# Optimization experiments

Hardware: AMD Instinct MI355X
Metric: run time of the kernel (lower is better)

## Reference

```python
import jax, jax.numpy as jnp
import numpy as np

EPS = 1e-12

def _l2norm(x):
    n = jnp.sqrt(jnp.sum(x * x, axis=-1, keepdims=True))
    return x / jnp.maximum(n, EPS)

def setup_inputs() -> dict:
    key = jax.random.key(0)
    k1, k2 = jax.random.split(key)
    B, S, H = 32, 256, 768
    return {
        "query_embs": jax.random.normal(k1, (B, S, H), dtype=jnp.float32),
        "key_embs": jax.random.normal(k2, (B, S, H), dtype=jnp.float32),
        "q_mask": jnp.ones((B, S), dtype=jnp.float32),
        "k_mask": jnp.ones((B, S), dtype=jnp.float32),
        "alpha_raw": jnp.asarray(1.0, dtype=jnp.float32),
        "logit_scale": jnp.asarray(0.0, dtype=jnp.float32),  # log(1.0)
    }

def reference(query_embs, key_embs, q_mask, k_mask, alpha_raw, logit_scale):
    # query_embs, key_embs: (B, S, H); masks: (B, S)
    S = query_embs.shape[1]
    q = _l2norm(query_embs)
    k = _l2norm(key_embs)
    # all-pairs token similarity: (B, B, S, T)
    sim = jnp.einsum('ish,jth->ijst', q, k)
    # distance-decay weighting (do_distance=True, exp_decay=True)
    alpha = jax.nn.softplus(alpha_raw)
    pos = jnp.arange(S, dtype=jnp.float32)
    dist = jnp.abs(pos[:, None] - pos[None, :])  # (S, S)
    sim = sim * jnp.exp(-alpha * dist)
    # validity mask: (B, B, S, T)
    valid = (q_mask[:, None, :, None] * k_mask[None, :, None, :]) > 0
    scale = jnp.exp(logit_scale)
    neg_inf = jnp.float32(-jnp.inf)
    logits = jnp.where(valid, scale * sim, neg_inf)
    all_inf = jnp.all(logits == neg_inf, axis=-1, keepdims=True)
    safe_logits = jnp.where(all_inf, 0.0, logits)
    p = jax.nn.softmax(safe_logits, axis=-1)
    p = jnp.where(all_inf, 0.0, p)
    # softmax-weighted key aggregation: (B, B, S, H)
    agg = jnp.einsum('ijst,jth->ijsh', p, k)
    # per-token cosine score, masked mean over query tokens
    scores = jnp.einsum('ish,ijsh->ijs', q, agg) * q_mask[:, None, :]
    denom = jnp.clip(jnp.sum(q_mask, axis=-1, keepdims=True), 1.0, None)
    return jnp.sum(scores, axis=-1) / denom  # (B, B)
```

## Files before the change

kernel.cpp:

```cpp
#include <hip/hip_runtime.h>
#include <cmath>

#define BB 32
#define SS 256
#define HH 768

typedef __attribute__((ext_vector_type(8))) short bfrag8;
typedef __attribute__((ext_vector_type(4))) float accf4;

__device__ __forceinline__ unsigned short f2bf(float x) {
    unsigned int b = __float_as_uint(x);
    return (unsigned short)((b + 0x7FFFu + ((b >> 16) & 1u)) >> 16);
}


__global__ __launch_bounds__(256)
void zero_kernel(float* __restrict__ Ksum) {
    Ksum[blockIdx.x * 256 + threadIdx.x] = 0.f;
}

__global__ __launch_bounds__(256)
void normcvt_kernel(const float* __restrict__ Q, const float* __restrict__ K,
                    const float* __restrict__ kmask,
                    float* __restrict__ invq, float* __restrict__ invk,
                    unsigned short* __restrict__ qws, unsigned short* __restrict__ kws,
                    float* __restrict__ Ksum) {
    __shared__ float sK[4 * HH];
    const int wave = threadIdx.x >> 6, lane = threadIdx.x & 63;
    const bool isQ = blockIdx.x < 2048;
    const int rr = (blockIdx.x * 4 + wave) & 8191;
    const float4* src4 = isQ ? (const float4*)(Q + (size_t)rr * HH)
                             : (const float4*)(K + (size_t)rr * HH);
    float4 vv[3]; float s = 0.f;
#pragma unroll
    for (int c = 0; c < 3; ++c) {
        vv[c] = src4[lane + 64 * c];
        s += vv[c].x * vv[c].x + vv[c].y * vv[c].y + vv[c].z * vv[c].z + vv[c].w * vv[c].w;
    }
#pragma unroll
    for (int off = 1; off < 64; off <<= 1) s += __shfl_xor(s, off);
    float inv = 1.f / fmaxf(sqrtf(s), 1e-12f);
    if (lane == 0) (isQ ? invq : invk)[rr] = inv;

    const int b = rr >> 8, srow = rr & 255;
    unsigned short* dst = isQ ? qws : kws;
    float m = 0.f;
    if (!isQ) m = (kmask[b * SS + srow] > 0.f) ? 1.f : 0.f;
    const int fp8 = (((((lane & 7) >> 1)) ^ ((srow >> 1) & 3)) << 3) + (lane & 1) * 4;
#pragma unroll
    for (int c = 0; c < 3; ++c) {
        int kc = (lane >> 3) + 8 * c;
        float4 n4;
        n4.x = vv[c].x * inv; n4.y = vv[c].y * inv; n4.z = vv[c].z * inv; n4.w = vv[c].w * inv;
        ushort4 o;
        o.x = f2bf(n4.x); o.y = f2bf(n4.y); o.z = f2bf(n4.z); o.w = f2bf(n4.w);
        *(ushort4*)(dst + (((size_t)b * 24 + kc) * 256 + srow) * 32 + fp8) = o;
        if (!isQ)
            *(float4*)(sK + wave * HH + (lane + 64 * c) * 4) =
                make_float4(n4.x * m, n4.y * m, n4.z * m, n4.w * m);
    }
    if (!isQ) {
        __syncthreads();
        const int j = ((int)blockIdx.x - 2048) >> 6;
        for (int e = threadIdx.x; e < HH; e += 256) {
            float v = sK[e] + sK[HH + e] + sK[2 * HH + e] + sK[3 * HH + e];
            atomicAdd(&Ksum[j * HH + e], v);
        }
    }
}

__global__ __launch_bounds__(256, 3)
void mfma_kernel(const unsigned short* __restrict__ qws, const unsigned short* __restrict__ kws,
                 const float* __restrict__ qmask, const float* __restrict__ kmask,
                 const float* __restrict__ araw_p, const float* __restrict__ lscale_p,
                 const float* __restrict__ Ksum, float* __restrict__ out) {
    __shared__ short lq[8192];
    __shared__ short lk[8192];
    __shared__ short lKsum[768];
    __shared__ float sKm[256];
    __shared__ float wtab[13];
    __shared__ float sRed[4][2];
    __shared__ float sPart[4];
    __shared__ float sKcnt, sQden;

    const int tid = threadIdx.x;
    const int lane = tid & 63, w = tid >> 6;
    const int quad = lane >> 4, col = lane & 15;
    const int i = blockIdx.x >> 5, j = blockIdx.x & 31;

    const float alpha = log1pf(__expf(araw_p[0]));
    const float scale = __expf(lscale_p[0]);

    float aq = qmask[i * SS + tid];
    float km = kmask[j * SS + tid];
    sKm[tid] = km;
    float c = (km > 0.f) ? 1.f : 0.f;
#pragma unroll
    for (int off = 1; off < 64; off <<= 1) { aq += __shfl_xor(aq, off); c += __shfl_xor(c, off); }
    if (lane == 0) { sRed[w][0] = aq; sRed[w][1] = c; }
    if (tid < 13) wtab[tid] = __expf(-alpha * (float)tid);
    if (tid < 192) {
        float4 kv = ((const float4*)(Ksum + (size_t)j * HH))[tid];
        ushort4 o;
        o.x = f2bf(kv.x); o.y = f2bf(kv.y); o.z = f2bf(kv.z); o.w = f2bf(kv.w);
        ((ushort4*)lKsum)[tid] = o;
    }
    __syncthreads();
    if (tid == 0) {
        sQden = fmaxf(sRed[0][0] + sRed[1][0] + sRed[2][0] + sRed[3][0], 1.f);
        sKcnt = sRed[0][1] + sRed[1][1] + sRed[2][1] + sRed[3][1];
    }

    accf4 acc[4][3];
    accf4 accB[4];
#pragma unroll
    for (int a = 0; a < 4; ++a) {
        accB[a] = (accf4)0.f;
#pragma unroll
        for (int b = 0; b < 3; ++b) acc[a][b] = (accf4)0.f;
    }

    const size_t qb0 = (size_t)i * 24 * 8192;
    const size_t kb0 = (size_t)j * 24 * 8192;
    const int perm8 = ((quad ^ ((col >> 1) & 3)) << 3);
    const unsigned short* qsrc = qws + qb0 + w * 2048 + lane * 8;
    const unsigned short* ksrc = kws + kb0 + w * 2048 + lane * 8;
    unsigned short* lqd = (unsigned short*)lq + w * 2048 + lane * 8;
    unsigned short* lkd = (unsigned short*)lk + w * 2048 + lane * 8;

    bfrag8 pq[4], pk[4];
#pragma unroll
    for (int n = 0; n < 4; ++n) {
        pq[n] = *(const bfrag8*)(qsrc + n * 512);
        pk[n] = *(const bfrag8*)(ksrc + n * 512);
    }

    for (int kc = 0; kc < 24; ++kc) {
        __syncthreads();
#pragma unroll
        for (int n = 0; n < 4; ++n) {
            *(bfrag8*)(lqd + n * 512) = pq[n];
            *(bfrag8*)(lkd + n * 512) = pk[n];
        }
        {
            const size_t noff = (size_t)((kc < 23) ? kc + 1 : 23) * 8192;
#pragma unroll
            for (int n = 0; n < 4; ++n) {
                pq[n] = *(const bfrag8*)(qsrc + noff + n * 512);
                pk[n] = *(const bfrag8*)(ksrc + noff + n * 512);
            }
        }
        __syncthreads();

        const bfrag8 kfrag = *(const bfrag8*)(lKsum + kc * 32 + quad * 8);
        bfrag8 bfr[6];
#pragma unroll
        for (int u = 0; u < 6; ++u) {
            int tb = 4 * w - 1 + u;
            if (tb >= 0 && tb <= 15)
                bfr[u] = *(const bfrag8*)(lk + (size_t)(tb * 16 + col) * 32 + perm8);
        }
#pragma unroll
        for (int sbl = 0; sbl < 4; ++sbl) {
            bfrag8 af = *(const bfrag8*)(lq + (size_t)((4 * w + sbl) * 16 + col) * 32 + perm8);
            accB[sbl] = __builtin_amdgcn_mfma_f32_16x16x32_bf16(af, kfrag, accB[sbl], 0, 0, 0);
#pragma unroll
            for (int dtb = 0; dtb < 3; ++dtb) {
                int tb = 4 * w + sbl - 1 + dtb;
                if (tb >= 0 && tb <= 15)
                    acc[sbl][dtb] = __builtin_amdgcn_mfma_f32_16x16x32_bf16(
                        af, bfr[sbl + dtb], acc[sbl][dtb], 0, 0, 0);
            }
        }
    }

    __syncthreads();
    const float kcnt = sKcnt;
    float part = 0.f;
#pragma unroll
    for (int sbl = 0; sbl < 4; ++sbl) {
        const int sbase = (4 * w + sbl) * 16 + quad * 4;
        float ns[4] = {0.f, 0.f, 0.f, 0.f}, ds[4] = {0.f, 0.f, 0.f, 0.f};
#pragma unroll
        for (int dtb = 0; dtb < 3; ++dtb) {
            int tb = 4 * w + sbl - 1 + dtb;
            if (tb < 0 || tb > 15) continue;
            int t = tb * 16 + col;
            float kmv = sKm[t];
#pragma unroll
            for (int reg = 0; reg < 4; ++reg) {
                int st = sbase + reg;
                int d = t - st;
                bool ok = (d >= -11) && (d <= 12) && (kmv > 0.f);
                int idx = d < 0 ? -d : d;
                idx = ok ? idx : 0;
                float raw = acc[sbl][dtb][reg];
                float e = ok ? expm1f(scale * raw * wtab[idx]) : 0.f;
                ns[reg] = fmaf(e, raw, ns[reg]);
                ds[reg] += e;
            }
        }
#pragma unroll
        for (int off = 1; off < 16; off <<= 1) {
#pragma unroll
            for (int reg = 0; reg < 4; ++reg) {
                ns[reg] += __shfl_xor(ns[reg], off);
                ds[reg] += __shfl_xor(ds[reg], off);
            }
        }
        if (col == 0) {
#pragma unroll
            for (int reg = 0; reg < 4; ++reg) {
                int st = sbase + reg;
                float qm = qmask[i * SS + st];
                float bse = accB[sbl][reg];
                float dtot = ds[reg] + kcnt;
                float v = (qm > 0.f && kcnt > 0.f) ? qm * (ns[reg] + bse) / dtot : 0.f;
                part += v;
            }
        }
    }
    part += __shfl_xor(part, 16);
    part += __shfl_xor(part, 32);
    if (lane == 0) sPart[w] = part;
    __syncthreads();
    if (tid == 0) out[i * BB + j] = (sPart[0] + sPart[1] + sPart[2] + sPart[3]) / sQden;
}


extern "C" void kernel_launch(void* const* d_in, const int* in_sizes, int n_in,
                              void* d_out, int out_size, void* d_ws, size_t ws_size,
                              hipStream_t stream) {
    const float* Q      = (const float*)d_in[0];
    const float* K      = (const float*)d_in[1];
    const float* qmask  = (const float*)d_in[2];
    const float* kmask  = (const float*)d_in[3];
    const float* araw   = (const float*)d_in[4];
    const float* lscale = (const float*)d_in[5];
    float* outp = (float*)d_out;

    float* invq  = (float*)d_ws;
    float* invk  = invq + 8192;
    float* Ksum  = invk + 8192;
    unsigned short* qws = (unsigned short*)(Ksum + 24576);
    unsigned short* kws = qws + 6291456;

    zero_kernel<<<96, 256, 0, stream>>>(Ksum);
    normcvt_kernel<<<4096, 256, 0, stream>>>(Q, K, kmask, invq, invk, qws, kws, Ksum);
    mfma_kernel<<<1024, 256, 0, stream>>>(qws, kws, qmask, kmask, araw, lscale, Ksum, outp);
}
```

Before: 163.2 us.

## Load MFMA fragments directly from global memory, dropping LDS staging

```diff
diff --git a/kernel.cpp b/kernel.cpp
--- a/kernel.cpp
+++ b/kernel.cpp
@@ -46,7 +46,7 @@
     unsigned short* dst = isQ ? qws : kws;
     float m = 0.f;
     if (!isQ) m = (kmask[b * SS + srow] > 0.f) ? 1.f : 0.f;
-    const int fp8 = (((((lane & 7) >> 1)) ^ ((srow >> 1) & 3)) << 3) + (lane & 1) * 4;
+    const int fp8 = (lane & 7) * 4;
 #pragma unroll
     for (int c = 0; c < 3; ++c) {
         int kc = (lane >> 3) + 8 * c;
@@ -73,9 +73,8 @@
 void mfma_kernel(const unsigned short* __restrict__ qws, const unsigned short* __restrict__ kws,
                  const float* __restrict__ qmask, const float* __restrict__ kmask,
                  const float* __restrict__ araw_p, const float* __restrict__ lscale_p,
-                 const float* __restrict__ Ksum, float* __restrict__ out) {
-    __shared__ short lq[8192];
-    __shared__ short lk[8192];
+                 const float* __restrict__ Ksum, const unsigned short* __restrict__ zpg,
+                 float* __restrict__ out) {
     __shared__ short lKsum[768];
     __shared__ float sKm[256];
     __shared__ float wtab[13];
@@ -120,58 +119,48 @@
         for (int b = 0; b < 3; ++b) acc[a][b] = (accf4)0.f;
     }
 
-    const size_t qb0 = (size_t)i * 24 * 8192;
-    const size_t kb0 = (size_t)j * 24 * 8192;
-    const int perm8 = ((quad ^ ((col >> 1) & 3)) << 3);
-    const unsigned short* qsrc = qws + qb0 + w * 2048 + lane * 8;
-    const unsigned short* ksrc = kws + kb0 + w * 2048 + lane * 8;
-    unsigned short* lqd = (unsigned short*)lq + w * 2048 + lane * 8;
-    unsigned short* lkd = (unsigned short*)lk + w * 2048 + lane * 8;
-
-    bfrag8 pq[4], pk[4];
-#pragma unroll
-    for (int n = 0; n < 4; ++n) {
-        pq[n] = *(const bfrag8*)(qsrc + n * 512);
-        pk[n] = *(const bfrag8*)(ksrc + n * 512);
-    }
-
+    const int lo = col * 32 + quad * 8;
+    const unsigned short* qp = qws + (size_t)i * 24 * 8192 + (4 * w) * 512 + lo;
+    const unsigned short* kb[6];
+    int kstep[6];
+#pragma unroll
+    for (int u = 0; u < 6; ++u) {
+        int tb = 4 * w - 1 + u;
+        bool inb = (tb >= 0) && (tb <= 15);
+        kb[u] = inb ? (kws + (size_t)j * 24 * 8192 + tb * 512 + lo) : (zpg + lo);
+        kstep[u] = inb ? 8192 : 0;
+    }
+
+    bfrag8 cq[4], ck[6];
+#pragma unroll
+    for (int n = 0; n < 4; ++n) cq[n] = *(const bfrag8*)(qp + n * 512);
+#pragma unroll
+    for (int u = 0; u < 6; ++u) ck[u] = *(const bfrag8*)(kb[u]);
+
+#pragma unroll
     for (int kc = 0; kc < 24; ++kc) {
-        __syncthreads();
-#pragma unroll
-        for (int n = 0; n < 4; ++n) {
-            *(bfrag8*)(lqd + n * 512) = pq[n];
-            *(bfrag8*)(lkd + n * 512) = pk[n];
-        }
-        {
-            const size_t noff = (size_t)((kc < 23) ? kc + 1 : 23) * 8192;
-#pragma unroll
-            for (int n = 0; n < 4; ++n) {
-                pq[n] = *(const bfrag8*)(qsrc + noff + n * 512);
-                pk[n] = *(const bfrag8*)(ksrc + noff + n * 512);
-            }
-        }
-        __syncthreads();
+        const int kn = (kc < 23) ? kc + 1 : 23;
+        bfrag8 nq[4], nk[6];
+#pragma unroll
+        for (int n = 0; n < 4; ++n)
+            nq[n] = *(const bfrag8*)(qp + (size_t)kn * 8192 + n * 512);
+#pragma unroll
+        for (int u = 0; u < 6; ++u)
+            nk[u] = *(const bfrag8*)(kb[u] + (size_t)kn * (size_t)kstep[u]);
 
         const bfrag8 kfrag = *(const bfrag8*)(lKsum + kc * 32 + quad * 8);
-        bfrag8 bfr[6];
-#pragma unroll
-        for (int u = 0; u < 6; ++u) {
-            int tb = 4 * w - 1 + u;
-            if (tb >= 0 && tb <= 15)
-                bfr[u] = *(const bfrag8*)(lk + (size_t)(tb * 16 + col) * 32 + perm8);
-        }
 #pragma unroll
         for (int sbl = 0; sbl < 4; ++sbl) {
-            bfrag8 af = *(const bfrag8*)(lq + (size_t)((4 * w + sbl) * 16 + col) * 32 + perm8);
-            accB[sbl] = __builtin_amdgcn_mfma_f32_16x16x32_bf16(af, kfrag, accB[sbl], 0, 0, 0);
-#pragma unroll
-            for (int dtb = 0; dtb < 3; ++dtb) {
-                int tb = 4 * w + sbl - 1 + dtb;
-                if (tb >= 0 && tb <= 15)
-                    acc[sbl][dtb] = __builtin_amdgcn_mfma_f32_16x16x32_bf16(
-                        af, bfr[sbl + dtb], acc[sbl][dtb], 0, 0, 0);
-            }
-        }
+            accB[sbl] = __builtin_amdgcn_mfma_f32_16x16x32_bf16(cq[sbl], kfrag, accB[sbl], 0, 0, 0);
+#pragma unroll
+            for (int dtb = 0; dtb < 3; ++dtb)
+                acc[sbl][dtb] = __builtin_amdgcn_mfma_f32_16x16x32_bf16(
+                    cq[sbl], ck[sbl + dtb], acc[sbl][dtb], 0, 0, 0);
+        }
+#pragma unroll
+        for (int n = 0; n < 4; ++n) cq[n] = nq[n];
+#pragma unroll
+        for (int u = 0; u < 6; ++u) ck[u] = nk[u];
     }
 
     __syncthreads();
@@ -242,10 +231,12 @@
     float* invq  = (float*)d_ws;
     float* invk  = invq + 8192;
     float* Ksum  = invk + 8192;
-    unsigned short* qws = (unsigned short*)(Ksum + 24576);
+    float* zpgf  = Ksum + 24576;
+    unsigned short* qws = (unsigned short*)(zpgf + 256);
     unsigned short* kws = qws + 6291456;
 
-    zero_kernel<<<96, 256, 0, stream>>>(Ksum);
+    zero_kernel<<<97, 256, 0, stream>>>(Ksum);
     normcvt_kernel<<<4096, 256, 0, stream>>>(Q, K, kmask, invq, invk, qws, kws, Ksum);
-    mfma_kernel<<<1024, 256, 0, stream>>>(qws, kws, qmask, kmask, araw, lscale, Ksum, outp);
-}
+    mfma_kernel<<<1024, 256, 0, stream>>>(qws, kws, qmask, kmask, araw, lscale,
+                                          Ksum, (const unsigned short*)zpgf, outp);
+}
```

Measured after the change: 188.0 us. 1.15x slower.

## Double-buffer LDS tiles with direct global-to-LDS loads in MFMA kernel

Applied to the files above, without the earlier changes.

```diff
diff --git a/kernel.cpp b/kernel.cpp
--- a/kernel.cpp
+++ b/kernel.cpp
@@ -11,6 +11,11 @@
 __device__ __forceinline__ unsigned short f2bf(float x) {
     unsigned int b = __float_as_uint(x);
     return (unsigned short)((b + 0x7FFFu + ((b >> 16) & 1u)) >> 16);
+}
+
+__device__ __forceinline__ void gload16(const void* g, void* l) {
+    __builtin_amdgcn_global_load_lds((const __attribute__((address_space(1))) void*)g,
+                                     (__attribute__((address_space(3))) void*)l, 16, 0, 0);
 }
 
 
@@ -69,13 +74,13 @@
     }
 }
 
-__global__ __launch_bounds__(256, 3)
+__global__ __launch_bounds__(256, 2)
 void mfma_kernel(const unsigned short* __restrict__ qws, const unsigned short* __restrict__ kws,
                  const float* __restrict__ qmask, const float* __restrict__ kmask,
                  const float* __restrict__ araw_p, const float* __restrict__ lscale_p,
                  const float* __restrict__ Ksum, float* __restrict__ out) {
-    __shared__ short lq[8192];
-    __shared__ short lk[8192];
+    __shared__ short lq[2][8192];
+    __shared__ short lk[2][8192];
     __shared__ short lKsum[768];
     __shared__ float sKm[256];
     __shared__ float wtab[13];
@@ -105,64 +110,61 @@
         o.x = f2bf(kv.x); o.y = f2bf(kv.y); o.z = f2bf(kv.z); o.w = f2bf(kv.w);
         ((ushort4*)lKsum)[tid] = o;
     }
+
+    accf4 acc[4][3];
+    accf4 accB[4];
+#pragma unroll
+    for (int a = 0; a < 4; ++a) {
+        accB[a] = (accf4)0.f;
+#pragma unroll
+        for (int b = 0; b < 3; ++b) acc[a][b] = (accf4)0.f;
+    }
+
+    const unsigned short* qsrc = qws + (size_t)i * 24 * 8192 + w * 2048 + lane * 8;
+    const unsigned short* ksrc = kws + (size_t)j * 24 * 8192 + w * 2048 + lane * 8;
+    const int perm8 = ((quad ^ ((col >> 1) & 3)) << 3);
+
+    {
+        unsigned short* lqd = (unsigned short*)&lq[0][0] + w * 2048;
+        unsigned short* lkd = (unsigned short*)&lk[0][0] + w * 2048;
+#pragma unroll
+        for (int n = 0; n < 4; ++n) {
+            gload16(qsrc + n * 512, lqd + n * 512);
+            gload16(ksrc + n * 512, lkd + n * 512);
+        }
+    }
     __syncthreads();
     if (tid == 0) {
         sQden = fmaxf(sRed[0][0] + sRed[1][0] + sRed[2][0] + sRed[3][0], 1.f);
         sKcnt = sRed[0][1] + sRed[1][1] + sRed[2][1] + sRed[3][1];
     }
 
-    accf4 acc[4][3];
-    accf4 accB[4];
-#pragma unroll
-    for (int a = 0; a < 4; ++a) {
-        accB[a] = (accf4)0.f;
-#pragma unroll
-        for (int b = 0; b < 3; ++b) acc[a][b] = (accf4)0.f;
-    }
-
-    const size_t qb0 = (size_t)i * 24 * 8192;
-    const size_t kb0 = (size_t)j * 24 * 8192;
-    const int perm8 = ((quad ^ ((col >> 1) & 3)) << 3);
-    const unsigned short* qsrc = qws + qb0 + w * 2048 + lane * 8;
-    const unsigned short* ksrc = kws + kb0 + w * 2048 + lane * 8;
-    unsigned short* lqd = (unsigned short*)lq + w * 2048 + lane * 8;
-    unsigned short* lkd = (unsigned short*)lk + w * 2048 + lane * 8;
-
-    bfrag8 pq[4], pk[4];
-#pragma unroll
-    for (int n = 0; n < 4; ++n) {
-        pq[n] = *(const bfrag8*)(qsrc + n * 512);
-        pk[n] = *(const bfrag8*)(ksrc + n * 512);
-    }
-
     for (int kc = 0; kc < 24; ++kc) {
-        __syncthreads();
-#pragma unroll
-        for (int n = 0; n < 4; ++n) {
-            *(bfrag8*)(lqd + n * 512) = pq[n];
-            *(bfrag8*)(lkd + n * 512) = pk[n];
-        }
-        {
-            const size_t noff = (size_t)((kc < 23) ? kc + 1 : 23) * 8192;
+        if (kc) __syncthreads();
+        if (kc < 23) {
+            const size_t o = (size_t)(kc + 1) * 8192;
+            unsigned short* lqd = (unsigned short*)&lq[(kc + 1) & 1][0] + w * 2048;
+            unsigned short* lkd = (unsigned short*)&lk[(kc + 1) & 1][0] + w * 2048;
 #pragma unroll
             for (int n = 0; n < 4; ++n) {
-                pq[n] = *(const bfrag8*)(qsrc + noff + n * 512);
-                pk[n] = *(const bfrag8*)(ksrc + noff + n * 512);
-            }
-        }
-        __syncthreads();
-
+                gload16(qsrc + o + n * 512, lqd + n * 512);
+                gload16(ksrc + o + n * 512, lkd + n * 512);
+            }
+        }
+
+        const short* lqc = &lq[kc & 1][0];
+        const short* lkc = &lk[kc & 1][0];
         const bfrag8 kfrag = *(const bfrag8*)(lKsum + kc * 32 + quad * 8);
         bfrag8 bfr[6];
 #pragma unroll
         for (int u = 0; u < 6; ++u) {
             int tb = 4 * w - 1 + u;
             if (tb >= 0 && tb <= 15)
-                bfr[u] = *(const bfrag8*)(lk + (size_t)(tb * 16 + col) * 32 + perm8);
+                bfr[u] = *(const bfrag8*)(lkc + (size_t)(tb * 16 + col) * 32 + perm8);
         }
 #pragma unroll
         for (int sbl = 0; sbl < 4; ++sbl) {
-            bfrag8 af = *(const bfrag8*)(lq + (size_t)((4 * w + sbl) * 16 + col) * 32 + perm8);
+            bfrag8 af = *(const bfrag8*)(lqc + (size_t)((4 * w + sbl) * 16 + col) * 32 + perm8);
             accB[sbl] = __builtin_amdgcn_mfma_f32_16x16x32_bf16(af, kfrag, accB[sbl], 0, 0, 0);
 #pragma unroll
             for (int dtb = 0; dtb < 3; ++dtb) {
```

Measured after the change: 212.8 us. +30.4%, slower.
